# Kernel tuning notes

Measured on AMD Instinct MI355X. Metric: run time of the kernel, lower is better.

The kernel has to match this reference:

```python
import jax, jax.numpy as jnp
import numpy as np

B, D, P, K, H = 8192, 64, 4, 16, 5
IN = D * P  # 256
NEG_SLOPE = 0.2
EPS = 1e-6  # GaussianNLLLoss var clamp


def setup_inputs() -> dict:
    key = jax.random.key(0)
    ks = jax.random.split(key, 13)
    s1 = 1.0 / np.sqrt(IN)
    s2 = 1.0 / np.sqrt(H + IN)
    return {
        "x_values": jax.random.normal(ks[0], (B, D), jnp.float32),
        "x_inputs": jax.random.normal(ks[1], (B, D, IN), jnp.float32),
        "targets": 0.1 * jax.random.normal(ks[2], (D, K, K - 1), jnp.float32),
        "W1": s1 * jax.random.normal(ks[3], (K, D, H, IN), jnp.float32),
        "b1": s1 * jax.random.normal(ks[4], (D, K, H), jnp.float32),
        "Wh": s2 * jax.random.normal(ks[5], (K, D, H), jnp.float32),
        "Wx": s2 * jax.random.normal(ks[6], (K, D, IN), jnp.float32),
        "b2": s2 * jax.random.normal(ks[7], (D, K), jnp.float32),
        "sW1": s1 * jax.random.normal(ks[8], (K, D, H, IN), jnp.float32),
        "sb1": s1 * jax.random.normal(ks[9], (D, K, H), jnp.float32),
        "sWh": s2 * jax.random.normal(ks[10], (K, D, H), jnp.float32),
        "sWx": s2 * jax.random.normal(ks[11], (K, D, IN), jnp.float32),
        "sb2": s2 * jax.random.normal(ks[12], (D, K), jnp.float32),
    }


def _grouped_mlp(x, W1, b1, Wh, Wx, b2):
    # x: (B, d, in); one tiny net per (k, j): Linear(in->H) + LeakyReLU,
    # then final Linear on concat([hidden, x]) (NO trailing activation; torch code uses net[-2]).
    h = jax.nn.leaky_relu(jnp.einsum('bji,kjhi->bjkh', x, W1) + b1, NEG_SLOPE)  # (B,d,K,H)
    out = (jnp.einsum('bjkh,kjh->bjk', h, Wh)
           + jnp.einsum('bji,kji->bjk', x, Wx)
           + b2)  # (B,d,K), out_dim=1 squeezed
    return out


def _target_weights(targets):
    # base[j,k,:] = [0, (targets*tril(-1))[j,k,:]] + eye(K)[k]
    tril = jnp.tril(jnp.ones((K, K - 1), jnp.float32), -1)  # (K, K-1)
    base = jnp.concatenate(
        [jnp.zeros((D, K, 1), targets.dtype), targets * tril], axis=2
    ) + jnp.eye(K, dtype=targets.dtype)  # (D, K, K)
    row_mask = jnp.tril(jnp.ones((K, K), jnp.float32))  # row k keeps cols 0..k
    logits = jnp.where(row_mask.astype(bool), base, -1e30)
    w = jax.nn.softmax(logits, axis=-1) * row_mask  # (D, K, K)
    return w


def reference(x_values, x_inputs, targets, W1, b1, Wh, Wx, b2,
              sW1, sb1, sWh, sWx, sb2):
    mean = _grouped_mlp(x_inputs, W1, b1, Wh, Wx, b2)      # (B,d,K)
    shared = _grouped_mlp(x_inputs, sW1, sb1, sWh, sWx, sb2)
    var = jnp.maximum((10.0 * jax.nn.sigmoid(shared)) ** 2, EPS)
    # GaussianNLLLoss(reduction='none'), full=False
    nll_node = 0.5 * (jnp.log(var) + (x_values[:, :, None] - mean) ** 2 / var)  # (B,d,K)
    w = _target_weights(targets)  # (d, K, K) row-masked softmax weights
    # nll[b,i] = sum_j sum_{k<=i} nll_node[b,j,k] * w[j,i,k]
    nll = jnp.einsum('bjk,jik->bi', nll_node, w)  # (B, K)
    return nll
```

## Files before the change

### kernel.cpp

```cpp
#include <hip/hip_runtime.h>

typedef float f32x4 __attribute__((ext_vector_type(4)));
typedef short bf16x8 __attribute__((ext_vector_type(8)));
typedef unsigned int u32x4 __attribute__((ext_vector_type(4)));

#define B_TOT 8192
#define D_ 64
#define K_ 16
#define H_ 5
#define IN_ 256

__device__ __forceinline__ unsigned short f2bf(float f){
  unsigned int u = __float_as_uint(f);
  u += 0x7fffu + ((u >> 16) & 1u);
  return (unsigned short)(u >> 16);
}

__device__ __forceinline__ unsigned int cvtpk(float lo, float hi){
  unsigned int r;
  asm("v_cvt_pk_bf16_f32 %0, %1, %2" : "=v"(r) : "v"(lo), "v"(hi));
  return r;
}

__global__ void pack_weights2_kernel(const float* __restrict__ W1,
                                     const float* __restrict__ Wx,
                                     const float* __restrict__ sW1,
                                     const float* __restrict__ sWx,
                                     unsigned short* __restrict__ Wpack2){
  int j = blockIdx.x, r = blockIdx.y, c = threadIdx.x;
  const float* src;
  if (r < 80)      { int k = r/5, h = r%5;             src = W1  + (((k*D_ + j)*H_ + h)*IN_); }
  else if (r < 96) { int k = r-80;                     src = Wx  + ((k*D_ + j)*IN_); }
  else if (r < 176){ int rr = r-96; int k=rr/5,h=rr%5; src = sW1 + (((k*D_ + j)*H_ + h)*IN_); }
  else             { int k = r-176;                    src = sWx + ((k*D_ + j)*IN_); }
  int kk = c >> 5, ks = (c >> 3) & 3, e = c & 7;
  Wpack2[((((size_t)j*8 + kk)*192 + r)*4 + ks)*8 + e] = f2bf(src[c]);
}

__global__ void pack_b1_kernel(const float* __restrict__ b1, const float* __restrict__ sb1,
                               float* __restrict__ b1pack){
  int j = blockIdx.x, r = threadIdx.x;
  float v = 0.f;
  if (r < 80) v = b1[j*80 + r];
  else if (r >= 96 && r < 176) v = sb1[j*80 + (r-96)];
  b1pack[j*192 + r] = v;
}

__global__ void pack_b2f_kernel(const float* __restrict__ Wh, const float* __restrict__ sWh,
                                unsigned short* __restrict__ B2packF){
  int j = blockIdx.x, kk = blockIdx.y, t = threadIdx.x;
  #pragma unroll
  for (int q = 0; q < 4; ++q){
    int f = t*4 + q;
    int e = f & 7, lg = (f >> 3) & 3, r = f >> 5;
    int c = kk*32 + lg*8 + e;
    int k = r & 15;
    int h = c - 5*k;
    float v = 0.f;
    if (h >= 0 && h < 5) v = (r < 16 ? Wh : sWh)[((size_t)k*D_ + j)*H_ + h];
    B2packF[((size_t)j*3 + kk)*1024 + f] = f2bf(v);
  }
}

__global__ void compute_w_kernel(const float* __restrict__ targets, float* __restrict__ wout){
  int j = blockIdx.x;
  int i = threadIdx.x;
  if (i >= K_) return;
  float base[K_];
  base[0] = (i == 0) ? 1.f : 0.f;
  for (int c = 1; c <= i; ++c)
    base[c] = targets[(j*K_ + i)*(K_-1) + (c-1)] + ((c == i) ? 1.f : 0.f);
  float mx = base[0];
  for (int c = 1; c <= i; ++c) mx = fmaxf(mx, base[c]);
  float e[K_]; float s = 0.f;
  for (int c = 0; c <= i; ++c){ e[c] = expf(base[c] - mx); s += e[c]; }
  float inv = 1.f / s;
  for (int c = 0; c < K_; ++c)
    wout[(j*K_ + i)*K_ + c] = (c <= i) ? e[c]*inv : 0.f;
}

__global__ __launch_bounds__(256, 3)
void main_kernel(const float* __restrict__ x_values,
                 const float* __restrict__ x_inputs,
                 const unsigned short* __restrict__ Wpack2,
                 const float* __restrict__ wsm,
                 const float* __restrict__ b1pack,
                 const unsigned short* __restrict__ B2packF,
                 const float* __restrict__ b2, const float* __restrict__ sb2,
                 float* __restrict__ partial){
  __shared__ __align__(16) char sm[53248];
  unsigned short* G = (unsigned short*)(sm + 16384);
  float* Gx  = (float*)(sm + 41984);
  float* Gsx = (float*)(sm + 47104);
  float* w_l = (float*)(sm + 52224);

  const int t   = threadIdx.x;
  const int lane = t & 63, wv = t >> 6;
  const int l15 = lane & 15, lg = lane >> 4;
  const int jg = blockIdx.x, b0 = blockIdx.y * 64;

  f32x4 acc1[4][3];
  f32x4 acc3 = {0.f,0.f,0.f,0.f};
  bf16x8 bfr[12];
  bf16x8 b2tf[6];

  for (int jj = 0; jj < 4; ++jj){
    const int j = jg*4 + jj;

    #pragma unroll
    for (int kkl = 0; kkl < 4; ++kkl)
      #pragma unroll
      for (int n = 0; n < 3; ++n){
        const int o = wv*48 + n*16 + l15;
        bfr[kkl*3+n] = *(const bf16x8*)(Wpack2 + ((((size_t)j*8 + kkl)*192 + o)*4 + lg)*8);
      }
    #pragma unroll
    for (int kk = 0; kk < 3; ++kk){
      b2tf[kk]   = *(const bf16x8*)(B2packF + ((size_t)j*3 + kk)*1024 + l15*32 + lg*8);
      b2tf[3+kk] = *(const bf16x8*)(B2packF + ((size_t)j*3 + kk)*1024 + (16+l15)*32 + lg*8);
    }
    w_l[t] = wsm[(j << 8) + t];

    {
      const int r0 = t >> 4, cb = t & 15;
      const float* ap = x_inputs + ((size_t)(b0 + r0)*D_ + j)*IN_ + cb*8;
      #pragma unroll
      for (int pp = 0; pp < 2; ++pp){
        f32x4 v[4];
        #pragma unroll
        for (int p = 0; p < 2; ++p){
          v[p*2]   = *(const f32x4*)(ap + (size_t)(pp*2+p)*16*D_*IN_);
          v[p*2+1] = *(const f32x4*)(ap + (size_t)(pp*2+p)*16*D_*IN_ + 4);
        }
        #pragma unroll
        for (int p = 0; p < 2; ++p){
          const int row = (pp*2+p)*16 + r0;
          u32x4 o;
          o[0] = cvtpk(v[p*2][0],   v[p*2][1]);
          o[1] = cvtpk(v[p*2][2],   v[p*2][3]);
          o[2] = cvtpk(v[p*2+1][0], v[p*2+1][1]);
          o[3] = cvtpk(v[p*2+1][2], v[p*2+1][3]);
          *(u32x4*)(sm + row*256 + ((cb*16) ^ ((row & 7) << 4))) = o;
        }
      }
    }
    #pragma unroll
    for (int m = 0; m < 4; ++m)
      #pragma unroll
      for (int n = 0; n < 3; ++n) acc1[m][n] = (f32x4){0.f,0.f,0.f,0.f};
    __syncthreads();

    #pragma unroll
    for (int kkl = 0; kkl < 4; ++kkl){
      bf16x8 af[4];
      #pragma unroll
      for (int m = 0; m < 4; ++m){
        const int row = m*16 + l15;
        af[m] = *(const bf16x8*)(sm + row*256 + ((kkl*64 + lg*16) ^ ((row & 7) << 4)));
      }
      #pragma unroll
      for (int m = 0; m < 4; ++m)
        #pragma unroll
        for (int n = 0; n < 3; ++n)
          acc1[m][n] = __builtin_amdgcn_mfma_f32_16x16x32_bf16(af[m], bfr[kkl*3+n], acc1[m][n], 0, 0, 0);
    }

    #pragma unroll
    for (int kkl = 0; kkl < 4; ++kkl)
      #pragma unroll
      for (int n = 0; n < 3; ++n){
        const int o = wv*48 + n*16 + l15;
        bfr[kkl*3+n] = *(const bf16x8*)(Wpack2 + ((((size_t)j*8 + 4 + kkl)*192 + o)*4 + lg)*8);
      }
    __syncthreads();

    {
      const int r0 = t >> 4, cb = t & 15;
      const float* ap = x_inputs + ((size_t)(b0 + r0)*D_ + j)*IN_ + 128 + cb*8;
      #pragma unroll
      for (int pp = 0; pp < 2; ++pp){
        f32x4 v[4];
        #pragma unroll
        for (int p = 0; p < 2; ++p){
          v[p*2]   = *(const f32x4*)(ap + (size_t)(pp*2+p)*16*D_*IN_);
          v[p*2+1] = *(const f32x4*)(ap + (size_t)(pp*2+p)*16*D_*IN_ + 4);
        }
        #pragma unroll
        for (int p = 0; p < 2; ++p){
          const int row = (pp*2+p)*16 + r0;
          u32x4 o;
          o[0] = cvtpk(v[p*2][0],   v[p*2][1]);
          o[1] = cvtpk(v[p*2][2],   v[p*2][3]);
          o[2] = cvtpk(v[p*2+1][0], v[p*2+1][1]);
          o[3] = cvtpk(v[p*2+1][2], v[p*2+1][3]);
          *(u32x4*)(sm + row*256 + ((cb*16) ^ ((row & 7) << 4))) = o;
        }
      }
    }
    __syncthreads();

    #pragma unroll
    for (int kkl = 0; kkl < 4; ++kkl){
      bf16x8 af[4];
      #pragma unroll
      for (int m = 0; m < 4; ++m){
        const int row = m*16 + l15;
        af[m] = *(const bf16x8*)(sm + row*256 + ((kkl*64 + lg*16) ^ ((row & 7) << 4)));
      }
      #pragma unroll
      for (int m = 0; m < 4; ++m)
        #pragma unroll
        for (int n = 0; n < 3; ++n)
          acc1[m][n] = __builtin_amdgcn_mfma_f32_16x16x32_bf16(af[m], bfr[kkl*3+n], acc1[m][n], 0, 0, 0);
    }

    #pragma unroll
    for (int n = 0; n < 3; ++n){
      const int col = wv*48 + n*16 + l15;
      const bool isx  = (col >= 80 && col < 96);
      const bool issx = (col >= 176);
      const float b1v = (isx || issx) ? 0.f : b1pack[j*192 + col];
      #pragma unroll
      for (int m = 0; m < 4; ++m){
        const int row = m*16 + lg*4;
        if (isx){
          #pragma unroll
          for (int e = 0; e < 4; ++e){
            Gx[(row+e)*20 + (col-80)] = acc1[m][n][e];
            G[(row+e)*200 + col] = 0;
          }
        } else if (issx){
          #pragma unroll
          for (int e = 0; e < 4; ++e){
            Gsx[(row+e)*20 + (col-176)] = acc1[m][n][e];
            G[(row+e)*200 + col] = 0;
          }
        } else {
          #pragma unroll
          for (int e = 0; e < 4; ++e){
            float v = acc1[m][n][e] + b1v;
            v = fmaxf(v, 0.2f*v);
            G[(row+e)*200 + col] = f2bf(v);
          }
        }
      }
    }
    __syncthreads();

    {
      const int brow = wv*16 + l15;
      f32x4 accm = *(const f32x4*)(Gx  + brow*20 + lg*4) + *(const f32x4*)(b2  + j*16 + lg*4);
      f32x4 accs = *(const f32x4*)(Gsx + brow*20 + lg*4) + *(const f32x4*)(sb2 + j*16 + lg*4);
      #pragma unroll
      for (int kk = 0; kk < 3; ++kk){
        bf16x8 g0 = *(const bf16x8*)((char*)G + brow*400       + kk*64 + lg*16);
        bf16x8 g1 = *(const bf16x8*)((char*)G + brow*400 + 192 + kk*64 + lg*16);
        accm = __builtin_amdgcn_mfma_f32_16x16x32_bf16(b2tf[kk],   g0, accm, 0, 0, 0);
        accs = __builtin_amdgcn_mfma_f32_16x16x32_bf16(b2tf[3+kk], g1, accs, 0, 0, 0);
      }

      const float xv = x_values[(size_t)(b0 + brow)*D_ + j];
      float nn4[4];
      #pragma unroll
      for (int e = 0; e < 4; ++e){
        float mean = accm[e];
        float shv  = accs[e];
        float ex = __expf(-shv);
        float sg = __fdividef(10.f, 1.f + ex);
        float var = fmaxf(sg*sg, 1e-6f);
        float d = xv - mean;
        nn4[e] = 0.5f*(__logf(var) + __fdividef(d*d, var));
      }

      #pragma unroll
      for (int g = 0; g < 4; ++g){
        float v0 = nn4[0], v1 = nn4[1], v2 = nn4[2], v3 = nn4[3];
        if (g){
          v0 = __shfl_xor(v0, g<<4); v1 = __shfl_xor(v1, g<<4);
          v2 = __shfl_xor(v2, g<<4); v3 = __shfl_xor(v3, g<<4);
        }
        const int kb = ((lg ^ g) << 2);
        #pragma unroll
        for (int q = 0; q < 4; ++q){
          f32x4 wq = *(const f32x4*)(w_l + (lg*4+q)*16 + kb);
          acc3[q] += wq[0]*v0 + wq[1]*v1 + wq[2]*v2 + wq[3]*v3;
        }
      }
    }
    __syncthreads();
  }

  *(f32x4*)(partial + ((size_t)jg*B_TOT + b0 + wv*16 + l15)*16 + lg*4) = acc3;
}

__global__ void reduce_kernel(const float* __restrict__ partial, float* __restrict__ out){
  int idx = blockIdx.x*256 + threadIdx.x;
  float s = 0.f;
  #pragma unroll
  for (int g = 0; g < 16; ++g) s += partial[(size_t)g*(B_TOT*K_) + idx];
  out[idx] = s;
}

extern "C" void kernel_launch(void* const* d_in, const int* in_sizes, int n_in,
                              void* d_out, int out_size, void* d_ws, size_t ws_size,
                              hipStream_t stream){
  const float* x_values = (const float*)d_in[0];
  const float* x_inputs = (const float*)d_in[1];
  const float* targets  = (const float*)d_in[2];
  const float* W1  = (const float*)d_in[3];
  const float* b1  = (const float*)d_in[4];
  const float* Wh  = (const float*)d_in[5];
  const float* Wx  = (const float*)d_in[6];
  const float* b2  = (const float*)d_in[7];
  const float* sW1 = (const float*)d_in[8];
  const float* sb1 = (const float*)d_in[9];
  const float* sWh = (const float*)d_in[10];
  const float* sWx = (const float*)d_in[11];
  const float* sb2 = (const float*)d_in[12];
  (void)in_sizes; (void)n_in; (void)out_size; (void)ws_size;

  char* ws = (char*)d_ws;
  unsigned short* Wpack2 = (unsigned short*)ws;
  float* wsm     = (float*)(ws + 6291456);
  float* b1pack  = (float*)(ws + 6356992);
  unsigned short* B2packF = (unsigned short*)(ws + 6406144);
  float* partial = (float*)(ws + 6799360);
  float* out = (float*)d_out;

  pack_weights2_kernel<<<dim3(64, 192), 256, 0, stream>>>(W1, Wx, sW1, sWx, Wpack2);
  pack_b1_kernel<<<dim3(64), 192, 0, stream>>>(b1, sb1, b1pack);
  pack_b2f_kernel<<<dim3(64, 3), 256, 0, stream>>>(Wh, sWh, B2packF);
  compute_w_kernel<<<dim3(64), 64, 0, stream>>>(targets, wsm);
  main_kernel<<<dim3(16, 128), 256, 0, stream>>>(x_values, x_inputs, Wpack2, wsm,
                                                 b1pack, B2packF, b2, sb2, partial);
  reduce_kernel<<<dim3(512), 256, 0, stream>>>(partial, out);
}
```

Before: 242.8 us.

## Restructure main kernel to per-wave row tiles with direct register A loads

Each wave now owns 16 batch rows and computes all 192 output columns, loading x_inputs straight into registers and converting to bf16 without staging through shared memory. This removes the block-wide __syncthreads and the LDS round-trip for the A operand. Weight fragments are instead streamed from global or L2 per MFMA, so weight traffic rises. The final weighted K-reduction becomes an f16 MFMA with a prepacked weight fragment, and blocks are remapped so the same j-group lands on the same XCD for L2 reuse.

```diff
diff --git a/kernel.cpp b/kernel.cpp
--- a/kernel.cpp
+++ b/kernel.cpp
@@ -3,6 +3,8 @@
 typedef float f32x4 __attribute__((ext_vector_type(4)));
 typedef short bf16x8 __attribute__((ext_vector_type(8)));
 typedef unsigned int u32x4 __attribute__((ext_vector_type(4)));
+typedef _Float16 f16x2 __attribute__((ext_vector_type(2)));
+typedef _Float16 f16x4 __attribute__((ext_vector_type(4)));
 
 #define B_TOT 8192
 #define D_ 64
@@ -62,7 +64,7 @@
   }
 }
 
-__global__ void compute_w_kernel(const float* __restrict__ targets, float* __restrict__ wout){
+__global__ void compute_w_kernel(const float* __restrict__ targets, _Float16* __restrict__ wf16){
   int j = blockIdx.x;
   int i = threadIdx.x;
   if (i >= K_) return;
@@ -75,222 +77,135 @@
   float e[K_]; float s = 0.f;
   for (int c = 0; c <= i; ++c){ e[c] = expf(base[c] - mx); s += e[c]; }
   float inv = 1.f / s;
-  for (int c = 0; c < K_; ++c)
-    wout[(j*K_ + i)*K_ + c] = (c <= i) ? e[c]*inv : 0.f;
+  for (int c = 0; c < K_; ++c){
+    float w = (c <= i) ? e[c]*inv : 0.f;
+    wf16[j*256 + ((c >> 2)*16 + i)*4 + (c & 3)] = (_Float16)w;
+  }
 }
 
 __global__ __launch_bounds__(256, 3)
 void main_kernel(const float* __restrict__ x_values,
                  const float* __restrict__ x_inputs,
                  const unsigned short* __restrict__ Wpack2,
-                 const float* __restrict__ wsm,
+                 const _Float16* __restrict__ wf16,
                  const float* __restrict__ b1pack,
                  const unsigned short* __restrict__ B2packF,
                  const float* __restrict__ b2, const float* __restrict__ sb2,
                  float* __restrict__ partial){
-  __shared__ __align__(16) char sm[53248];
-  unsigned short* G = (unsigned short*)(sm + 16384);
-  float* Gx  = (float*)(sm + 41984);
-  float* Gsx = (float*)(sm + 47104);
-  float* w_l = (float*)(sm + 52224);
-
-  const int t   = threadIdx.x;
+  __shared__ __align__(16) char sm[35840];
+
+  const int t    = threadIdx.x;
   const int lane = t & 63, wv = t >> 6;
-  const int l15 = lane & 15, lg = lane >> 4;
-  const int jg = blockIdx.x, b0 = blockIdx.y * 64;
-
-  f32x4 acc1[4][3];
+  const int l15  = lane & 15, lg = lane >> 4;
+
+  const int bx  = blockIdx.x;
+  const int xcd = bx & 7, q8 = bx >> 3;
+  const int bt  = q8 & 127, jg = xcd*2 + (q8 >> 7);
+  const int b0  = bt * 64;
+
+  char* Gw = sm + wv*8960;
+  unsigned short* G = (unsigned short*)Gw;
+  float* Gx  = (float*)(Gw + 6656);
+  float* Gsx = (float*)(Gw + 7744);
+
+  const int myrow = b0 + wv*16 + l15;
+
   f32x4 acc3 = {0.f,0.f,0.f,0.f};
-  bf16x8 bfr[12];
-  bf16x8 b2tf[6];
 
   for (int jj = 0; jj < 4; ++jj){
     const int j = jg*4 + jj;
 
+    const f16x4 wfrag = *(const f16x4*)(wf16 + j*256 + lane*4);
+
+    f32x4 acc1[12];
     #pragma unroll
-    for (int kkl = 0; kkl < 4; ++kkl)
-      #pragma unroll
-      for (int n = 0; n < 3; ++n){
-        const int o = wv*48 + n*16 + l15;
-        bfr[kkl*3+n] = *(const bf16x8*)(Wpack2 + ((((size_t)j*8 + kkl)*192 + o)*4 + lg)*8);
-      }
+    for (int n = 0; n < 12; ++n) acc1[n] = (f32x4){0.f,0.f,0.f,0.f};
+
+    const float* aprow = x_inputs + ((size_t)myrow*D_ + j)*IN_;
+
     #pragma unroll
-    for (int kk = 0; kk < 3; ++kk){
-      b2tf[kk]   = *(const bf16x8*)(B2packF + ((size_t)j*3 + kk)*1024 + l15*32 + lg*8);
-      b2tf[3+kk] = *(const bf16x8*)(B2packF + ((size_t)j*3 + kk)*1024 + (16+l15)*32 + lg*8);
+    for (int kc = 0; kc < 2; ++kc){
+      f32x4 av[8];
+      #pragma unroll
+      for (int kkl = 0; kkl < 4; ++kkl){
+        av[kkl*2]   = *(const f32x4*)(aprow + kc*128 + kkl*32 + lg*8);
+        av[kkl*2+1] = *(const f32x4*)(aprow + kc*128 + kkl*32 + lg*8 + 4);
+      }
+      #pragma unroll
+      for (int kkl = 0; kkl < 4; ++kkl){
+        u32x4 at;
+        at[0] = cvtpk(av[kkl*2][0],   av[kkl*2][1]);
+        at[1] = cvtpk(av[kkl*2][2],   av[kkl*2][3]);
+        at[2] = cvtpk(av[kkl*2+1][0], av[kkl*2+1][1]);
+        at[3] = cvtpk(av[kkl*2+1][2], av[kkl*2+1][3]);
+        const bf16x8 af = __builtin_bit_cast(bf16x8, at);
+        const unsigned short* wp = Wpack2 + (size_t)(j*8 + kc*4 + kkl)*6144 + l15*32 + lg*8;
+        #pragma unroll
+        for (int n = 0; n < 12; ++n){
+          bf16x8 bfr = *(const bf16x8*)(wp + n*512);
+          acc1[n] = __builtin_amdgcn_mfma_f32_16x16x32_bf16(af, bfr, acc1[n], 0, 0, 0);
+        }
+      }
     }
-    w_l[t] = wsm[(j << 8) + t];
+
+    #pragma unroll
+    for (int n = 0; n < 12; ++n){
+      if (n == 5){
+        #pragma unroll
+        for (int e = 0; e < 4; ++e){
+          Gx[(lg*4+e)*17 + l15] = acc1[5][e];
+          G[(lg*4+e)*208 + 80 + l15] = 0;
+        }
+      } else if (n == 11){
+        #pragma unroll
+        for (int e = 0; e < 4; ++e){
+          Gsx[(lg*4+e)*17 + l15] = acc1[11][e];
+          G[(lg*4+e)*208 + 176 + l15] = 0;
+        }
+      } else {
+        const float b1v = b1pack[j*192 + n*16 + l15];
+        #pragma unroll
+        for (int e = 0; e < 4; ++e){
+          float v = acc1[n][e] + b1v;
+          v = fmaxf(v, 0.2f*v);
+          G[(lg*4+e)*208 + n*16 + l15] = f2bf(v);
+        }
+      }
+    }
 
     {
-      const int r0 = t >> 4, cb = t & 15;
-      const float* ap = x_inputs + ((size_t)(b0 + r0)*D_ + j)*IN_ + cb*8;
-      #pragma unroll
-      for (int pp = 0; pp < 2; ++pp){
-        f32x4 v[4];
-        #pragma unroll
-        for (int p = 0; p < 2; ++p){
-          v[p*2]   = *(const f32x4*)(ap + (size_t)(pp*2+p)*16*D_*IN_);
-          v[p*2+1] = *(const f32x4*)(ap + (size_t)(pp*2+p)*16*D_*IN_ + 4);
-        }
-        #pragma unroll
-        for (int p = 0; p < 2; ++p){
-          const int row = (pp*2+p)*16 + r0;
-          u32x4 o;
-          o[0] = cvtpk(v[p*2][0],   v[p*2][1]);
-          o[1] = cvtpk(v[p*2][2],   v[p*2][3]);
-          o[2] = cvtpk(v[p*2+1][0], v[p*2+1][1]);
-          o[3] = cvtpk(v[p*2+1][2], v[p*2+1][3]);
-          *(u32x4*)(sm + row*256 + ((cb*16) ^ ((row & 7) << 4))) = o;
-        }
-      }
-    }
-    #pragma unroll
-    for (int m = 0; m < 4; ++m)
-      #pragma unroll
-      for (int n = 0; n < 3; ++n) acc1[m][n] = (f32x4){0.f,0.f,0.f,0.f};
-    __syncthreads();
-
-    #pragma unroll
-    for (int kkl = 0; kkl < 4; ++kkl){
-      bf16x8 af[4];
-      #pragma unroll
-      for (int m = 0; m < 4; ++m){
-        const int row = m*16 + l15;
-        af[m] = *(const bf16x8*)(sm + row*256 + ((kkl*64 + lg*16) ^ ((row & 7) << 4)));
-      }
-      #pragma unroll
-      for (int m = 0; m < 4; ++m)
-        #pragma unroll
-        for (int n = 0; n < 3; ++n)
-          acc1[m][n] = __builtin_amdgcn_mfma_f32_16x16x32_bf16(af[m], bfr[kkl*3+n], acc1[m][n], 0, 0, 0);
-    }
-
-    #pragma unroll
-    for (int kkl = 0; kkl < 4; ++kkl)
-      #pragma unroll
-      for (int n = 0; n < 3; ++n){
-        const int o = wv*48 + n*16 + l15;
-        bfr[kkl*3+n] = *(const bf16x8*)(Wpack2 + ((((size_t)j*8 + 4 + kkl)*192 + o)*4 + lg)*8);
-      }
-    __syncthreads();
-
-    {
-      const int r0 = t >> 4, cb = t & 15;
-      const float* ap = x_inputs + ((size_t)(b0 + r0)*D_ + j)*IN_ + 128 + cb*8;
-      #pragma unroll
-      for (int pp = 0; pp < 2; ++pp){
-        f32x4 v[4];
-        #pragma unroll
-        for (int p = 0; p < 2; ++p){
-          v[p*2]   = *(const f32x4*)(ap + (size_t)(pp*2+p)*16*D_*IN_);
-          v[p*2+1] = *(const f32x4*)(ap + (size_t)(pp*2+p)*16*D_*IN_ + 4);
-        }
-        #pragma unroll
-        for (int p = 0; p < 2; ++p){
-          const int row = (pp*2+p)*16 + r0;
-          u32x4 o;
-          o[0] = cvtpk(v[p*2][0],   v[p*2][1]);
-          o[1] = cvtpk(v[p*2][2],   v[p*2][3]);
-          o[2] = cvtpk(v[p*2+1][0], v[p*2+1][1]);
-          o[3] = cvtpk(v[p*2+1][2], v[p*2+1][3]);
-          *(u32x4*)(sm + row*256 + ((cb*16) ^ ((row & 7) << 4))) = o;
-        }
-      }
-    }
-    __syncthreads();
-
-    #pragma unroll
-    for (int kkl = 0; kkl < 4; ++kkl){
-      bf16x8 af[4];
-      #pragma unroll
-      for (int m = 0; m < 4; ++m){
-        const int row = m*16 + l15;
-        af[m] = *(const bf16x8*)(sm + row*256 + ((kkl*64 + lg*16) ^ ((row & 7) << 4)));
-      }
-      #pragma unroll
-      for (int m = 0; m < 4; ++m)
-        #pragma unroll
-        for (int n = 0; n < 3; ++n)
-          acc1[m][n] = __builtin_amdgcn_mfma_f32_16x16x32_bf16(af[m], bfr[kkl*3+n], acc1[m][n], 0, 0, 0);
-    }
-
-    #pragma unroll
-    for (int n = 0; n < 3; ++n){
-      const int col = wv*48 + n*16 + l15;
-      const bool isx  = (col >= 80 && col < 96);
-      const bool issx = (col >= 176);
-      const float b1v = (isx || issx) ? 0.f : b1pack[j*192 + col];
-      #pragma unroll
-      for (int m = 0; m < 4; ++m){
-        const int row = m*16 + lg*4;
-        if (isx){
-          #pragma unroll
-          for (int e = 0; e < 4; ++e){
-            Gx[(row+e)*20 + (col-80)] = acc1[m][n][e];
-            G[(row+e)*200 + col] = 0;
-          }
-        } else if (issx){
-          #pragma unroll
-          for (int e = 0; e < 4; ++e){
-            Gsx[(row+e)*20 + (col-176)] = acc1[m][n][e];
-            G[(row+e)*200 + col] = 0;
-          }
-        } else {
-          #pragma unroll
-          for (int e = 0; e < 4; ++e){
-            float v = acc1[m][n][e] + b1v;
-            v = fmaxf(v, 0.2f*v);
-            G[(row+e)*200 + col] = f2bf(v);
-          }
-        }
-      }
-    }
-    __syncthreads();
-
-    {
-      const int brow = wv*16 + l15;
-      f32x4 accm = *(const f32x4*)(Gx  + brow*20 + lg*4) + *(const f32x4*)(b2  + j*16 + lg*4);
-      f32x4 accs = *(const f32x4*)(Gsx + brow*20 + lg*4) + *(const f32x4*)(sb2 + j*16 + lg*4);
+      f32x4 accm = *(const f32x4*)(Gx  + l15*17 + lg*4) + *(const f32x4*)(b2  + j*16 + lg*4);
+      f32x4 accs = *(const f32x4*)(Gsx + l15*17 + lg*4) + *(const f32x4*)(sb2 + j*16 + lg*4);
       #pragma unroll
       for (int kk = 0; kk < 3; ++kk){
-        bf16x8 g0 = *(const bf16x8*)((char*)G + brow*400       + kk*64 + lg*16);
-        bf16x8 g1 = *(const bf16x8*)((char*)G + brow*400 + 192 + kk*64 + lg*16);
-        accm = __builtin_amdgcn_mfma_f32_16x16x32_bf16(b2tf[kk],   g0, accm, 0, 0, 0);
-        accs = __builtin_amdgcn_mfma_f32_16x16x32_bf16(b2tf[3+kk], g1, accs, 0, 0, 0);
-      }
-
-      const float xv = x_values[(size_t)(b0 + brow)*D_ + j];
+        bf16x8 a0 = *(const bf16x8*)(B2packF + ((size_t)j*3 + kk)*1024 + l15*32 + lg*8);
+        bf16x8 a1 = *(const bf16x8*)(B2packF + ((size_t)j*3 + kk)*1024 + (16+l15)*32 + lg*8);
+        bf16x8 g0 = *(const bf16x8*)((char*)G + l15*416       + kk*64 + lg*16);
+        bf16x8 g1 = *(const bf16x8*)((char*)G + l15*416 + 192 + kk*64 + lg*16);
+        accm = __builtin_amdgcn_mfma_f32_16x16x32_bf16(a0, g0, accm, 0, 0, 0);
+        accs = __builtin_amdgcn_mfma_f32_16x16x32_bf16(a1, g1, accs, 0, 0, 0);
+      }
+
+      const float xv = x_values[(size_t)myrow*D_ + j];
       float nn4[4];
       #pragma unroll
       for (int e = 0; e < 4; ++e){
         float mean = accm[e];
         float shv  = accs[e];
-        float ex = __expf(-shv);
-        float sg = __fdividef(10.f, 1.f + ex);
-        float var = fmaxf(sg*sg, 1e-6f);
-        float d = xv - mean;
+        float sg   = __fdividef(10.f, 1.f + __expf(-shv));
+        float var  = fmaxf(sg*sg, 1e-6f);
+        float d    = xv - mean;
         nn4[e] = 0.5f*(__logf(var) + __fdividef(d*d, var));
       }
 
-      #pragma unroll
-      for (int g = 0; g < 4; ++g){
-        float v0 = nn4[0], v1 = nn4[1], v2 = nn4[2], v3 = nn4[3];
-        if (g){
-          v0 = __shfl_xor(v0, g<<4); v1 = __shfl_xor(v1, g<<4);
-          v2 = __shfl_xor(v2, g<<4); v3 = __shfl_xor(v3, g<<4);
-        }
-        const int kb = ((lg ^ g) << 2);
-        #pragma unroll
-        for (int q = 0; q < 4; ++q){
-          f32x4 wq = *(const f32x4*)(w_l + (lg*4+q)*16 + kb);
-          acc3[q] += wq[0]*v0 + wq[1]*v1 + wq[2]*v2 + wq[3]*v3;
-        }
-      }
+      f16x2 p0 = __builtin_bit_cast(f16x2, __builtin_amdgcn_cvt_pkrtz(nn4[0], nn4[1]));
+      f16x2 p1 = __builtin_bit_cast(f16x2, __builtin_amdgcn_cvt_pkrtz(nn4[2], nn4[3]));
+      f16x4 nf = {p0[0], p0[1], p1[0], p1[1]};
+      acc3 = __builtin_amdgcn_mfma_f32_16x16x16f16(wfrag, nf, acc3, 0, 0, 0);
     }
-    __syncthreads();
   }
 
-  *(f32x4*)(partial + ((size_t)jg*B_TOT + b0 + wv*16 + l15)*16 + lg*4) = acc3;
+  *(f32x4*)(partial + ((size_t)jg*B_TOT + myrow)*K_ + lg*4) = acc3;
 }
 
 __global__ void reduce_kernel(const float* __restrict__ partial, float* __restrict__ out){
@@ -320,18 +235,18 @@
   (void)in_sizes; (void)n_in; (void)out_size; (void)ws_size;
 
   char* ws = (char*)d_ws;
-  unsigned short* Wpack2 = (unsigned short*)ws;
-  float* wsm     = (float*)(ws + 6291456);
-  float* b1pack  = (float*)(ws + 6356992);
-  unsigned short* B2packF = (unsigned short*)(ws + 6406144);
-  float* partial = (float*)(ws + 6799360);
+  unsigned short* Wpack2  = (unsigned short*)ws;
+  float* b1pack           = (float*)(ws + 6291456);
+  unsigned short* B2packF = (unsigned short*)(ws + 6340608);
+  _Float16* wf16          = (_Float16*)(ws + 6733824);
+  float* partial          = (float*)(ws + 6766592);
   float* out = (float*)d_out;
 
   pack_weights2_kernel<<<dim3(64, 192), 256, 0, stream>>>(W1, Wx, sW1, sWx, Wpack2);
   pack_b1_kernel<<<dim3(64), 192, 0, stream>>>(b1, sb1, b1pack);
   pack_b2f_kernel<<<dim3(64, 3), 256, 0, stream>>>(Wh, sWh, B2packF);
-  compute_w_kernel<<<dim3(64), 64, 0, stream>>>(targets, wsm);
-  main_kernel<<<dim3(16, 128), 256, 0, stream>>>(x_values, x_inputs, Wpack2, wsm,
-                                                 b1pack, B2packF, b2, sb2, partial);
+  compute_w_kernel<<<dim3(64), 64, 0, stream>>>(targets, wf16);
+  main_kernel<<<dim3(2048), 256, 0, stream>>>(x_values, x_inputs, Wpack2, wf16,
+                                              b1pack, B2packF, b2, sb2, partial);
   reduce_kernel<<<dim3(512), 256, 0, stream>>>(partial, out);
 }
```

Result: slower. 350.5 us (+44.4%).

## Software-pipeline x_inputs loads across K-chunks and use MFMA for weighted NLL sum

Applied to the files above, without the earlier changes.

The main loop is restructured so the global loads of the next x_inputs chunk, including the first chunk of the next j, are issued while the MFMAs on the current chunk run, with sched_barriers pinning the order. The softmax weights are packed as fp16 in MFMA fragment layout, and the final weighted reduction becomes a single 16x16x16 f16 MFMA instead of shuffles plus LDS reads. b1 values are preloaded into registers. The extra registers come with launch bounds lowered from 3 to 2 blocks per CU, which cuts occupancy. The NLL values and weights are also rounded to fp16, which loses some precision.

```diff
diff --git a/kernel.cpp b/kernel.cpp
--- a/kernel.cpp
+++ b/kernel.cpp
@@ -3,6 +3,8 @@
 typedef float f32x4 __attribute__((ext_vector_type(4)));
 typedef short bf16x8 __attribute__((ext_vector_type(8)));
 typedef unsigned int u32x4 __attribute__((ext_vector_type(4)));
+typedef _Float16 f16x2 __attribute__((ext_vector_type(2)));
+typedef _Float16 f16x4 __attribute__((ext_vector_type(4)));
 
 #define B_TOT 8192
 #define D_ 64
@@ -62,7 +64,7 @@
   }
 }
 
-__global__ void compute_w_kernel(const float* __restrict__ targets, float* __restrict__ wout){
+__global__ void compute_w_kernel(const float* __restrict__ targets, _Float16* __restrict__ wf16){
   int j = blockIdx.x;
   int i = threadIdx.x;
   if (i >= K_) return;
@@ -75,81 +77,84 @@
   float e[K_]; float s = 0.f;
   for (int c = 0; c <= i; ++c){ e[c] = expf(base[c] - mx); s += e[c]; }
   float inv = 1.f / s;
-  for (int c = 0; c < K_; ++c)
-    wout[(j*K_ + i)*K_ + c] = (c <= i) ? e[c]*inv : 0.f;
-}
-
-__global__ __launch_bounds__(256, 3)
+  for (int c = 0; c < K_; ++c){
+    float w = (c <= i) ? e[c]*inv : 0.f;
+    wf16[j*256 + ((c >> 2)*16 + i)*4 + (c & 3)] = (_Float16)w;
+  }
+}
+
+__global__ __launch_bounds__(256, 2)
 void main_kernel(const float* __restrict__ x_values,
                  const float* __restrict__ x_inputs,
                  const unsigned short* __restrict__ Wpack2,
-                 const float* __restrict__ wsm,
+                 const _Float16* __restrict__ wf16,
                  const float* __restrict__ b1pack,
                  const unsigned short* __restrict__ B2packF,
                  const float* __restrict__ b2, const float* __restrict__ sb2,
                  float* __restrict__ partial){
-  __shared__ __align__(16) char sm[53248];
+  __shared__ __align__(16) char sm[52224];
   unsigned short* G = (unsigned short*)(sm + 16384);
   float* Gx  = (float*)(sm + 41984);
   float* Gsx = (float*)(sm + 47104);
-  float* w_l = (float*)(sm + 52224);
-
-  const int t   = threadIdx.x;
+
+  const int t    = threadIdx.x;
   const int lane = t & 63, wv = t >> 6;
-  const int l15 = lane & 15, lg = lane >> 4;
+  const int l15  = lane & 15, lg = lane >> 4;
+  const int r0   = t >> 4, cb = t & 15;
   const int jg = blockIdx.x, b0 = blockIdx.y * 64;
 
-  f32x4 acc1[4][3];
-  f32x4 acc3 = {0.f,0.f,0.f,0.f};
+  f32x4  av[8];
   bf16x8 bfr[12];
-  bf16x8 b2tf[6];
+  f32x4  acc3 = {0.f,0.f,0.f,0.f};
+
+  auto issueA = [&](int j, int kc){
+    const float* ap = x_inputs + ((size_t)(b0 + r0)*D_ + j)*IN_ + kc*128 + cb*8;
+    #pragma unroll
+    for (int p = 0; p < 4; ++p){
+      av[p*2]   = *(const f32x4*)(ap + (size_t)p*16*D_*IN_);
+      av[p*2+1] = *(const f32x4*)(ap + (size_t)p*16*D_*IN_ + 4);
+    }
+  };
+  auto cvtWriteA = [&](){
+    #pragma unroll
+    for (int p = 0; p < 4; ++p){
+      const int row = p*16 + r0;
+      u32x4 o;
+      o[0] = cvtpk(av[p*2][0],   av[p*2][1]);
+      o[1] = cvtpk(av[p*2][2],   av[p*2][3]);
+      o[2] = cvtpk(av[p*2+1][0], av[p*2+1][1]);
+      o[3] = cvtpk(av[p*2+1][2], av[p*2+1][3]);
+      *(u32x4*)(sm + row*256 + ((cb*16) ^ ((row & 7) << 4))) = o;
+    }
+  };
+  auto issueB = [&](int j, int kc){
+    #pragma unroll
+    for (int kkl = 0; kkl < 4; ++kkl)
+      #pragma unroll
+      for (int n = 0; n < 3; ++n){
+        const int o = wv*48 + n*16 + l15;
+        bfr[kkl*3+n] = *(const bf16x8*)(Wpack2 + ((((size_t)j*8 + kc*4 + kkl)*192 + o)*4 + lg)*8);
+      }
+  };
+
+  issueA(jg*4, 0);
 
   for (int jj = 0; jj < 4; ++jj){
     const int j = jg*4 + jj;
 
-    #pragma unroll
-    for (int kkl = 0; kkl < 4; ++kkl)
-      #pragma unroll
-      for (int n = 0; n < 3; ++n){
-        const int o = wv*48 + n*16 + l15;
-        bfr[kkl*3+n] = *(const bf16x8*)(Wpack2 + ((((size_t)j*8 + kkl)*192 + o)*4 + lg)*8);
-      }
-    #pragma unroll
-    for (int kk = 0; kk < 3; ++kk){
-      b2tf[kk]   = *(const bf16x8*)(B2packF + ((size_t)j*3 + kk)*1024 + l15*32 + lg*8);
-      b2tf[3+kk] = *(const bf16x8*)(B2packF + ((size_t)j*3 + kk)*1024 + (16+l15)*32 + lg*8);
-    }
-    w_l[t] = wsm[(j << 8) + t];
-
-    {
-      const int r0 = t >> 4, cb = t & 15;
-      const float* ap = x_inputs + ((size_t)(b0 + r0)*D_ + j)*IN_ + cb*8;
-      #pragma unroll
-      for (int pp = 0; pp < 2; ++pp){
-        f32x4 v[4];
-        #pragma unroll
-        for (int p = 0; p < 2; ++p){
-          v[p*2]   = *(const f32x4*)(ap + (size_t)(pp*2+p)*16*D_*IN_);
-          v[p*2+1] = *(const f32x4*)(ap + (size_t)(pp*2+p)*16*D_*IN_ + 4);
-        }
-        #pragma unroll
-        for (int p = 0; p < 2; ++p){
-          const int row = (pp*2+p)*16 + r0;
-          u32x4 o;
-          o[0] = cvtpk(v[p*2][0],   v[p*2][1]);
-          o[1] = cvtpk(v[p*2][2],   v[p*2][3]);
-          o[2] = cvtpk(v[p*2+1][0], v[p*2+1][1]);
-          o[3] = cvtpk(v[p*2+1][2], v[p*2+1][3]);
-          *(u32x4*)(sm + row*256 + ((cb*16) ^ ((row & 7) << 4))) = o;
-        }
-      }
-    }
+    f32x4 acc1[4][3];
     #pragma unroll
     for (int m = 0; m < 4; ++m)
       #pragma unroll
       for (int n = 0; n < 3; ++n) acc1[m][n] = (f32x4){0.f,0.f,0.f,0.f};
+
+    issueB(j, 0);
+    __builtin_amdgcn_sched_barrier(0);
+    cvtWriteA();
     __syncthreads();
 
+    issueA(j, 1);
+    __builtin_amdgcn_sched_barrier(0);
     #pragma unroll
     for (int kkl = 0; kkl < 4; ++kkl){
       bf16x8 af[4];
@@ -164,41 +169,26 @@
         for (int n = 0; n < 3; ++n)
           acc1[m][n] = __builtin_amdgcn_mfma_f32_16x16x32_bf16(af[m], bfr[kkl*3+n], acc1[m][n], 0, 0, 0);
     }
-
-    #pragma unroll
-    for (int kkl = 0; kkl < 4; ++kkl)
-      #pragma unroll
-      for (int n = 0; n < 3; ++n){
-        const int o = wv*48 + n*16 + l15;
-        bfr[kkl*3+n] = *(const bf16x8*)(Wpack2 + ((((size_t)j*8 + 4 + kkl)*192 + o)*4 + lg)*8);
-      }
     __syncthreads();
 
-    {
-      const int r0 = t >> 4, cb = t & 15;
-      const float* ap = x_inputs + ((size_t)(b0 + r0)*D_ + j)*IN_ + 128 + cb*8;
-      #pragma unroll
-      for (int pp = 0; pp < 2; ++pp){
-        f32x4 v[4];
-        #pragma unroll
-        for (int p = 0; p < 2; ++p){
-          v[p*2]   = *(const f32x4*)(ap + (size_t)(pp*2+p)*16*D_*IN_);
-          v[p*2+1] = *(const f32x4*)(ap + (size_t)(pp*2+p)*16*D_*IN_ + 4);
-        }
-        #pragma unroll
-        for (int p = 0; p < 2; ++p){
-          const int row = (pp*2+p)*16 + r0;
-          u32x4 o;
-          o[0] = cvtpk(v[p*2][0],   v[p*2][1]);
-          o[1] = cvtpk(v[p*2][2],   v[p*2][3]);
-          o[2] = cvtpk(v[p*2+1][0], v[p*2+1][1]);
-          o[3] = cvtpk(v[p*2+1][2], v[p*2+1][3]);
-          *(u32x4*)(sm + row*256 + ((cb*16) ^ ((row & 7) << 4))) = o;
-        }
-      }
-    }
+    issueB(j, 1);
+    __builtin_amdgcn_sched_barrier(0);
+    cvtWriteA();
     __syncthreads();
 
+    bf16x8 b2tf[6];
+    f16x4  wfrag;
+    float  b1f[12];
+    if (jj < 3) issueA(j+1, 0);
+    #pragma unroll
+    for (int kk = 0; kk < 3; ++kk){
+      b2tf[kk]   = *(const bf16x8*)(B2packF + ((size_t)j*3 + kk)*1024 + l15*32 + lg*8);
+      b2tf[3+kk] = *(const bf16x8*)(B2packF + ((size_t)j*3 + kk)*1024 + (16+l15)*32 + lg*8);
+    }
+    wfrag = *(const f16x4*)(wf16 + j*256 + lane*4);
+    #pragma unroll
+    for (int n = 0; n < 12; ++n) b1f[n] = b1pack[j*192 + n*16 + l15];
+    __builtin_amdgcn_sched_barrier(0);
     #pragma unroll
     for (int kkl = 0; kkl < 4; ++kkl){
       bf16x8 af[4];
@@ -213,13 +203,12 @@
         for (int n = 0; n < 3; ++n)
           acc1[m][n] = __builtin_amdgcn_mfma_f32_16x16x32_bf16(af[m], bfr[kkl*3+n], acc1[m][n], 0, 0, 0);
     }
-
     #pragma unroll
     for (int n = 0; n < 3; ++n){
       const int col = wv*48 + n*16 + l15;
+      const int nid = wv*3 + n;
       const bool isx  = (col >= 80 && col < 96);
       const bool issx = (col >= 176);
-      const float b1v = (isx || issx) ? 0.f : b1pack[j*192 + col];
       #pragma unroll
       for (int m = 0; m < 4; ++m){
         const int row = m*16 + lg*4;
@@ -238,7 +227,7 @@
         } else {
           #pragma unroll
           for (int e = 0; e < 4; ++e){
-            float v = acc1[m][n][e] + b1v;
+            float v = acc1[m][n][e] + b1f[nid];
             v = fmaxf(v, 0.2f*v);
             G[(row+e)*200 + col] = f2bf(v);
           }
@@ -265,32 +254,20 @@
       for (int e = 0; e < 4; ++e){
         float mean = accm[e];
         float shv  = accs[e];
-        float ex = __expf(-shv);
-        float sg = __fdividef(10.f, 1.f + ex);
-        float var = fmaxf(sg*sg, 1e-6f);
-        float d = xv - mean;
+        float sg   = __fdividef(10.f, 1.f + __expf(-shv));
+        float var  = fmaxf(sg*sg, 1e-6f);
+        float d    = xv - mean;
         nn4[e] = 0.5f*(__logf(var) + __fdividef(d*d, var));
       }
 
-      #pragma unroll
-      for (int g = 0; g < 4; ++g){
-        float v0 = nn4[0], v1 = nn4[1], v2 = nn4[2], v3 = nn4[3];
-        if (g){
-          v0 = __shfl_xor(v0, g<<4); v1 = __shfl_xor(v1, g<<4);
-          v2 = __shfl_xor(v2, g<<4); v3 = __shfl_xor(v3, g<<4);
-        }
-        const int kb = ((lg ^ g) << 2);
-        #pragma unroll
-        for (int q = 0; q < 4; ++q){
-          f32x4 wq = *(const f32x4*)(w_l + (lg*4+q)*16 + kb);
-          acc3[q] += wq[0]*v0 + wq[1]*v1 + wq[2]*v2 + wq[3]*v3;
-        }
-      }
-    }
-    __syncthreads();
+      f16x2 p0 = __builtin_bit_cast(f16x2, __builtin_amdgcn_cvt_pkrtz(nn4[0], nn4[1]));
+      f16x2 p1 = __builtin_bit_cast(f16x2, __builtin_amdgcn_cvt_pkrtz(nn4[2], nn4[3]));
+      f16x4 nf = {p0[0], p0[1], p1[0], p1[1]};
+      acc3 = __builtin_amdgcn_mfma_f32_16x16x16f16(wfrag, nf, acc3, 0, 0, 0);
+    }
   }
 
-  *(f32x4*)(partial + ((size_t)jg*B_TOT + b0 + wv*16 + l15)*16 + lg*4) = acc3;
+  *(f32x4*)(partial + ((size_t)jg*B_TOT + b0 + wv*16 + l15)*K_ + lg*4) = acc3;
 }
 
 __global__ void reduce_kernel(const float* __restrict__ partial, float* __restrict__ out){
@@ -320,18 +297,18 @@
   (void)in_sizes; (void)n_in; (void)out_size; (void)ws_size;
 
   char* ws = (char*)d_ws;
-  unsigned short* Wpack2 = (unsigned short*)ws;
-  float* wsm     = (float*)(ws + 6291456);
-  float* b1pack  = (float*)(ws + 6356992);
-  unsigned short* B2packF = (unsigned short*)(ws + 6406144);
-  float* partial = (float*)(ws + 6799360);
+  unsigned short* Wpack2  = (unsigned short*)ws;
+  float* b1pack           = (float*)(ws + 6291456);
+  unsigned short* B2packF = (unsigned short*)(ws + 6340608);
+  _Float16* wf16          = (_Float16*)(ws + 6733824);
+  float* partial          = (float*)(ws + 6766592);
   float* out = (float*)d_out;
 
   pack_weights2_kernel<<<dim3(64, 192), 256, 0, stream>>>(W1, Wx, sW1, sWx, Wpack2);
   pack_b1_kernel<<<dim3(64), 192, 0, stream>>>(b1, sb1, b1pack);
   pack_b2f_kernel<<<dim3(64, 3), 256, 0, stream>>>(Wh, sWh, B2packF);
-  compute_w_kernel<<<dim3(64), 64, 0, stream>>>(targets, wsm);
-  main_kernel<<<dim3(16, 128), 256, 0, stream>>>(x_values, x_inputs, Wpack2, wsm,
+  compute_w_kernel<<<dim3(64), 64, 0, stream>>>(targets, wf16);
+  main_kernel<<<dim3(16, 128), 256, 0, stream>>>(x_values, x_inputs, Wpack2, wf16,
                                                  b1pack, B2packF, b2, sb2, partial);
   reduce_kernel<<<dim3(512), 256, 0, stream>>>(partial, out);
 }
```

Result: faster. 214.0 us (-11.8%).
